# Optimization experiments

Hardware: AMD Instinct MI355X
Metric: run time of the kernel (lower is better)

The kernel has to match this reference:

```python
import jax, jax.numpy as jnp
import numpy as np

B, N, T_IN, F_IN = 16, 30000, 6, 1
E = 120000          # edges per etype
N_ETYPES = 2        # etypes per graph (hg and tg each)
KT, LK = 3, 3
C1, C2 = 8, 11      # block channel sizes
HID = 128


def _conv2d(x, w, b):
    # x: [B,Cin,T,N], w: [Cout,Cin,kt,1] -> valid conv
    y = jax.lax.conv_general_dilated(x, w, window_strides=(1, 1), padding='VALID',
                                     dimension_numbers=('NCHW', 'OIHW', 'NCHW'))
    return y + b[None, :, None, None]


def _glu_tconv(x, w, b, c_out, x_align):
    # TemporalConvLayer with act='GLU'
    xc = _conv2d(x, w, b)
    return (xc[:, :c_out] + x_align) * jax.nn.sigmoid(xc[:, c_out:])


def _hetcheb(X, edges, W, bias):
    # Heterogeneous ChebConv (sum over edge types), lambda_max=2 => L_hat = -D^-1/2 A D^-1/2
    # X: [S,N,Cin], edges: [n_et,2,E] int32, W: [n_et,Lk,Cin,Cout], bias: [n_et,Cout]
    S, n, cin = X.shape
    Lk = W.shape[1]
    Xn = jnp.transpose(X, (1, 0, 2))  # [N,S,Cin]
    out = jnp.zeros((n, S, W.shape[-1]), X.dtype)
    for e in range(edges.shape[0]):
        src, dst = edges[e, 0], edges[e, 1]
        ones = jnp.ones(src.shape, X.dtype)
        deg_in = jnp.clip(jax.ops.segment_sum(ones, dst, num_segments=n), 1.0)
        deg_out = jnp.clip(jax.ops.segment_sum(ones, src, num_segments=n), 1.0)
        norm = jax.lax.rsqrt(deg_out)[src] * jax.lax.rsqrt(deg_in)[dst]  # [E]
        def prop(Tm):  # L_hat @ T = -(Ahat @ T); vectorized over all B*T slices at once
            Tf = Tm.reshape(n, S * cin)
            return -jax.ops.segment_sum(norm[:, None] * Tf[src], dst, num_segments=n).reshape(n, S, cin)
        Tkm2 = Xn
        Tkm1 = prop(Xn)
        z = jnp.einsum('nsc,cd->nsd', Tkm2, W[e, 0]) + jnp.einsum('nsc,cd->nsd', Tkm1, W[e, 1])
        for k in range(2, Lk):
            Tk = 2.0 * prop(Tkm1) - Tkm2
            z = z + jnp.einsum('nsc,cd->nsd', Tk, W[e, k])
            Tkm2, Tkm1 = Tkm1, Tk
        out = out + z + bias[e][None, None, :]
    return jnp.transpose(out, (1, 0, 2))  # [S,N,Cout]


def _block(x, hg_edges, tg_edges, align_fn, tw, tb, hW, hb, tW, tb2, c_out):
    # HetETAConvBlock (dropout = identity in eval)
    x_align = align_fn(x)[:, :, KT - 1:, :]
    x_t1 = _glu_tconv(x, tw, tb, c_out, x_align)          # [B,c_out,T',N]
    b_, c_, t_, n_ = x_t1.shape
    X = jnp.transpose(x_t1, (0, 2, 3, 1)).reshape(b_ * t_, n_, c_)  # batched slices
    xs = _hetcheb(X, hg_edges, hW, hb).reshape(b_, t_, n_, -1).transpose(0, 3, 1, 2)
    xt = _hetcheb(X, tg_edges, tW, tb2).reshape(b_, t_, n_, -1).transpose(0, 3, 1, 2)
    return jnp.concatenate([xs, xt], axis=1)              # [B,2*c_out,T',N]


def setup_inputs() -> dict:
    key = jax.random.key(0)
    ks = jax.random.split(key, 20)
    s = 0.1
    inp = {
        'x': jax.random.normal(ks[0], (B, N, T_IN, F_IN), jnp.float32),
        'hg_edges': jax.random.randint(ks[1], (N_ETYPES, 2, E), 0, N, jnp.int32),
        'tg_edges': jax.random.randint(ks[2], (N_ETYPES, 2, E), 0, N, jnp.int32),
        # block1: tconv GLU 1 -> 8 (out 2*8 channels)
        'tconv1_w': jax.random.normal(ks[3], (2 * C1, F_IN, KT, 1), jnp.float32) * s,
        'tconv1_b': jnp.zeros((2 * C1,), jnp.float32),
        'h1_W': jax.random.normal(ks[4], (N_ETYPES, LK, C1, C1), jnp.float32) * s,
        'h1_b': jnp.zeros((N_ETYPES, C1), jnp.float32),
        't1_W': jax.random.normal(ks[5], (N_ETYPES, LK, C1, C1), jnp.float32) * s,
        't1_b': jnp.zeros((N_ETYPES, C1), jnp.float32),
        # block2: align 16 -> 11 (conv1x1), tconv GLU 16 -> 11
        'align2_w': jax.random.normal(ks[6], (C2, 2 * C1, 1, 1), jnp.float32) * s,
        'align2_b': jnp.zeros((C2,), jnp.float32),
        'tconv2_w': jax.random.normal(ks[7], (2 * C2, 2 * C1, KT, 1), jnp.float32) * s,
        'tconv2_b': jnp.zeros((2 * C2,), jnp.float32),
        'h2_W': jax.random.normal(ks[8], (N_ETYPES, LK, C2, C2), jnp.float32) * s,
        'h2_b': jnp.zeros((N_ETYPES, C2), jnp.float32),
        't2_W': jax.random.normal(ks[9], (N_ETYPES, LK, C2, C2), jnp.float32) * s,
        't2_b': jnp.zeros((N_ETYPES, C2), jnp.float32),
        # output linear: 11*2*(6-2*(3-1)) = 44 -> HID
        'out_w': jax.random.normal(ks[10], (2 * C2 * (T_IN - 2 * (KT - 1)), HID), jnp.float32) * s,
        'out_b': jnp.zeros((HID,), jnp.float32),
    }
    return inp


def reference(x, hg_edges, tg_edges, tconv1_w, tconv1_b, h1_W, h1_b, t1_W, t1_b,
              align2_w, align2_b, tconv2_w, tconv2_b, h2_W, h2_b, t2_W, t2_b,
              out_w, out_b):
    x = jnp.transpose(x, (0, 3, 2, 1))  # [B,1,T,N]
    # block1: Align pads channels 1 -> 8
    align1 = lambda v: jnp.pad(v, ((0, 0), (0, C1 - F_IN), (0, 0), (0, 0)))
    x1 = _block(x, hg_edges, tg_edges, align1, tconv1_w, tconv1_b, h1_W, h1_b, t1_W, t1_b, C1)
    # block2: Align is 1x1 conv 16 -> 11
    align2 = lambda v: _conv2d(v, align2_w, align2_b)
    x2 = _block(x1, hg_edges, tg_edges, align2, tconv2_w, tconv2_b, h2_W, h2_b, t2_W, t2_b, C2)
    b_, c_, t_, n_ = x2.shape
    z = jnp.transpose(x2, (0, 3, 1, 2)).reshape(b_, n_, c_ * t_)  # [B,N,44]
    return z @ out_w + out_b  # [B,N,HID]
```

## Files before the change

### kernel.cpp

```cpp
#include <hip/hip_runtime.h>
#include <hip/hip_fp16.h>
#include <math.h>

#define EDGES 120000
#define NN    30000
#define NCH   118
#define T1SLOT 15360000

__device__ __forceinline__ float sigmoidf_(float x) { return 1.f / (1.f + __expf(-x)); }

union F4H8 { float4 v; __half h[8]; };
union F2H4 { float2 v; __half h[4]; };

__device__ __forceinline__ void unpack8(float4 v, float* f) {
  F4H8 u; u.v = v;
#pragma unroll
  for (int i = 0; i < 8; ++i) f[i] = __half2float(u.h[i]);
}
__device__ __forceinline__ float4 pack8(const float* f) {
  F4H8 u;
#pragma unroll
  for (int i = 0; i < 8; ++i) u.h[i] = __float2half(f[i]);
  return u.v;
}
__device__ __forceinline__ void unpack4(float2 v, float* f) {
  F2H4 u; u.v = v;
#pragma unroll
  for (int i = 0; i < 4; ++i) f[i] = __half2float(u.h[i]);
}
__device__ __forceinline__ float2 pack4(const float* f) {
  F2H4 u;
#pragma unroll
  for (int i = 0; i < 4; ++i) u.h[i] = __float2half(f[i]);
  return u.v;
}

#define CSR_STRIDE 270016
#define CSR_RP(base, l)   ((base) + (size_t)(l) * CSR_STRIDE)
#define CSR_PK(base, l)   ((const int2*)((base) + (size_t)(l) * CSR_STRIDE + 30016))
#define CSR_PKW(base, l)  ((int2*)((base) + (size_t)(l) * CSR_STRIDE + 30016))

__global__ void count_all_kernel(const int* __restrict__ hg, const int* __restrict__ tg,
                                 int* __restrict__ degO, int* __restrict__ degI) {
  int tid = blockIdx.x * blockDim.x + threadIdx.x;
  if (tid >= 4 * EDGES) return;
  int l = tid / EDGES, j = tid - l * EDGES;
  const int* G = (l < 2) ? hg : tg;
  const int* src = G + (size_t)(l & 1) * 2 * EDGES;
  const int* dst = src + EDGES;
  atomicAdd(&degO[l * NN + src[j]], 1);
  atomicAdd(&degI[l * NN + dst[j]], 1);
}

__global__ __launch_bounds__(256) void scan1_kernel(const int* __restrict__ degI,
                                                    int* __restrict__ csrBase,
                                                    int* __restrict__ partials) {
  int l = blockIdx.x / NCH, ch = blockIdx.x - l * NCH;
  int tid = threadIdx.x;
  int i = ch * 256 + tid;
  __shared__ int buf[256];
  int v = (i < NN) ? degI[l * NN + i] : 0;
  buf[tid] = v;
  __syncthreads();
  for (int off = 1; off < 256; off <<= 1) {
    int t = (tid >= off) ? buf[tid - off] : 0;
    __syncthreads();
    buf[tid] += t;
    __syncthreads();
  }
  int* rp = CSR_RP(csrBase, l);
  if (i < NN) rp[i + 1] = buf[tid];
  if (tid == 255) partials[l * NCH + ch] = buf[255];
}

__global__ __launch_bounds__(128) void scan2_kernel(int* __restrict__ partials) {
  __shared__ int buf[128];
  int tid = threadIdx.x;
  for (int l = 0; l < 4; ++l) {
    int v = (tid < NCH) ? partials[l * NCH + tid] : 0;
    buf[tid] = v;
    __syncthreads();
    for (int off = 1; off < 128; off <<= 1) {
      int t = (tid >= off) ? buf[tid - off] : 0;
      __syncthreads();
      buf[tid] += t;
      __syncthreads();
    }
    if (tid < NCH) partials[l * NCH + tid] = buf[tid] - v;
    __syncthreads();
  }
}

__global__ __launch_bounds__(256) void fixup_kernel(int* __restrict__ csrBase,
                                                    int* __restrict__ cursor,
                                                    const int* __restrict__ partials) {
  int l = blockIdx.x / NCH, ch = blockIdx.x - l * NCH;
  int i = ch * 256 + threadIdx.x;
  int* rp = CSR_RP(csrBase, l);
  int off = partials[l * NCH + ch];
  if (i < NN) {
    int val = rp[i + 1] + off;
    rp[i + 1] = val;
    if (i + 1 < NN) cursor[l * NN + i + 1] = val;
  }
  if (i == 0) { rp[0] = 0; cursor[l * NN] = 0; }
}

__global__ void fill_all_kernel(const int* __restrict__ hg, const int* __restrict__ tg,
                                const int* __restrict__ degO, const int* __restrict__ degI,
                                int* __restrict__ cursor, int* __restrict__ csrBase) {
  int tid = blockIdx.x * blockDim.x + threadIdx.x;
  if (tid >= 4 * EDGES) return;
  int l = tid / EDGES, j = tid - l * EDGES;
  const int* G = (l < 2) ? hg : tg;
  const int* src = G + (size_t)(l & 1) * 2 * EDGES;
  const int* dst = src + EDGES;
  int s = src[j], d = dst[j];
  int doo = degO[l * NN + s]; if (doo < 1) doo = 1;
  int dii = degI[l * NN + d]; if (dii < 1) dii = 1;
  float nm = rsqrtf((float)doo) * rsqrtf((float)dii);
  int p = atomicAdd(&cursor[l * NN + d], 1);
  CSR_PKW(csrBase, l)[p] = make_int2(s, __float_as_int(nm));
}

__global__ void glu1_kernel(const float* __restrict__ x, const float* __restrict__ w,
                            const float* __restrict__ b, __half* __restrict__ X1h) {
  int idx = blockIdx.x * blockDim.x + threadIdx.x;
  if (idx >= NN * 64) return;
  int n = idx >> 6, s = idx & 63;
  int bb = s >> 2, t = s & 3;
  const float* xb = x + ((long)bb * NN + n) * 6;
  float x0 = xb[t], x1 = xb[t + 1], x2 = xb[t + 2];
  float o[8];
#pragma unroll
  for (int c = 0; c < 8; ++c) {
    float p = w[c * 3 + 0] * x0 + w[c * 3 + 1] * x1 + w[c * 3 + 2] * x2 + b[c];
    float q = w[(c + 8) * 3 + 0] * x0 + w[(c + 8) * 3 + 1] * x1 + w[(c + 8) * 3 + 2] * x2 + b[c + 8];
    float al = (c == 0) ? x2 : 0.f;
    o[c] = (p + al) * sigmoidf_(q);
  }
  reinterpret_cast<float4*>(X1h)[idx] = pack8(o);
}

__global__ __launch_bounds__(256) void pull1_kernel(const int* __restrict__ csrBase,
                                                    const __half* __restrict__ Xh,
                                                    __half* __restrict__ T1hAll) {
  int gtid = blockIdx.x * 256 + threadIdx.x;
  int l = gtid / (NN * 64);
  int t = gtid - l * (NN * 64);
  int n = t >> 6, j = t & 63;
  const int* rp = CSR_RP(csrBase, l);
  const int2* pk = CSR_PK(csrBase, l);
  const float4* in4 = reinterpret_cast<const float4*>(Xh);
  float acc[8];
#pragma unroll
  for (int i = 0; i < 8; ++i) acc[i] = 0.f;
  int e = rp[n], end = rp[n + 1];
  for (; e + 4 <= end; e += 4) {
    int2 p0 = pk[e], p1 = pk[e + 1], p2 = pk[e + 2], p3 = pk[e + 3];
    float4 v0 = in4[(long)p0.x * 64 + j];
    float4 v1 = in4[(long)p1.x * 64 + j];
    float4 v2 = in4[(long)p2.x * 64 + j];
    float4 v3 = in4[(long)p3.x * 64 + j];
    float f[8];
    float n0 = __int_as_float(p0.y), n1 = __int_as_float(p1.y);
    float n2 = __int_as_float(p2.y), n3 = __int_as_float(p3.y);
    unpack8(v0, f);
#pragma unroll
    for (int i = 0; i < 8; ++i) acc[i] -= n0 * f[i];
    unpack8(v1, f);
#pragma unroll
    for (int i = 0; i < 8; ++i) acc[i] -= n1 * f[i];
    unpack8(v2, f);
#pragma unroll
    for (int i = 0; i < 8; ++i) acc[i] -= n2 * f[i];
    unpack8(v3, f);
#pragma unroll
    for (int i = 0; i < 8; ++i) acc[i] -= n3 * f[i];
  }
  for (; e < end; ++e) {
    int2 p = pk[e];
    float4 v = in4[(long)p.x * 64 + j];
    float nm = __int_as_float(p.y);
    float f[8];
    unpack8(v, f);
#pragma unroll
    for (int i = 0; i < 8; ++i) acc[i] -= nm * f[i];
  }
  reinterpret_cast<float4*>(T1hAll)[(size_t)l * (T1SLOT / 8) + t] = pack8(acc);
}

__global__ __launch_bounds__(256) void cheb1_kernel(const int* __restrict__ csrBase,
    const __half* __restrict__ Xh, const __half* __restrict__ T1hAll,
    const float* __restrict__ Whg, const float* __restrict__ bhg,
    const float* __restrict__ Wtg, const float* __restrict__ btg,
    __half* __restrict__ outH, __half* __restrict__ outT) {
  constexpr int C = 8, CC = 64;
  __shared__ float wx[CC], w1a[CC], w1b[CC], w2a[CC], w2b[CC], bs[C];
  int gtid = blockIdx.x * 256 + threadIdx.x;
  int g = gtid / (NN * 64);
  int tid = gtid - g * (NN * 64);
  const float* W = g ? Wtg : Whg;
  const float* bias = g ? btg : bhg;
  for (int i = threadIdx.x; i < CC; i += 256) {
    float w0A = W[i], w1A = W[CC + i], w2A = W[2 * CC + i];
    float w0B = W[3 * CC + i], w1B = W[4 * CC + i], w2B = W[5 * CC + i];
    wx[i] = w0A - w2A + w0B - w2B;
    w1a[i] = w1A; w1b[i] = w1B;
    w2a[i] = -2.f * w2A; w2b[i] = -2.f * w2B;
  }
  if (threadIdx.x < C) bs[threadIdx.x] = bias[threadIdx.x] + bias[C + threadIdx.x];
  __syncthreads();
  int n = tid >> 6, s = tid & 63;
  int l0 = 2 * g, l1 = 2 * g + 1;
  const int* rp0 = CSR_RP(csrBase, l0); const int2* pk0 = CSR_PK(csrBase, l0);
  const int* rp1 = CSR_RP(csrBase, l1); const int2* pk1 = CSR_PK(csrBase, l1);
  const float4* A4 = reinterpret_cast<const float4*>(T1hAll + (size_t)l0 * T1SLOT);
  const float4* B4 = reinterpret_cast<const float4*>(T1hAll + (size_t)l1 * T1SLOT);
  float acc0[C], acc1[C];
#pragma unroll
  for (int c = 0; c < C; ++c) { acc0[c] = 0.f; acc1[c] = 0.f; }
  {
    int e = rp0[n], end = rp0[n + 1];
    for (; e + 2 <= end; e += 2) {
      int2 p0 = pk0[e], p1 = pk0[e + 1];
      float4 v0 = A4[(long)p0.x * 64 + s];
      float4 v1 = A4[(long)p1.x * 64 + s];
      float n0 = __int_as_float(p0.y), n1 = __int_as_float(p1.y);
      float f0[8], f1[8];
      unpack8(v0, f0); unpack8(v1, f1);
#pragma unroll
      for (int c = 0; c < C; ++c) acc0[c] += n0 * f0[c] + n1 * f1[c];
    }
    for (; e < end; ++e) {
      int2 p = pk0[e];
      float4 v = A4[(long)p.x * 64 + s];
      float nm = __int_as_float(p.y);
      float f[8]; unpack8(v, f);
#pragma unroll
      for (int c = 0; c < C; ++c) acc0[c] += nm * f[c];
    }
  }
  {
    int e = rp1[n], end = rp1[n + 1];
    for (; e + 2 <= end; e += 2) {
      int2 p0 = pk1[e], p1 = pk1[e + 1];
      float4 v0 = B4[(long)p0.x * 64 + s];
      float4 v1 = B4[(long)p1.x * 64 + s];
      float n0 = __int_as_float(p0.y), n1 = __int_as_float(p1.y);
      float f0[8], f1[8];
      unpack8(v0, f0); unpack8(v1, f1);
#pragma unroll
      for (int c = 0; c < C; ++c) acc1[c] += n0 * f0[c] + n1 * f1[c];
    }
    for (; e < end; ++e) {
      int2 p = pk1[e];
      float4 v = B4[(long)p.x * 64 + s];
      float nm = __int_as_float(p.y);
      float f[8]; unpack8(v, f);
#pragma unroll
      for (int c = 0; c < C; ++c) acc1[c] += nm * f[c];
    }
  }
  float z[C];
#pragma unroll
  for (int d = 0; d < C; ++d) z[d] = bs[d];
  {
    float xv[8], av[8], bv[8];
    unpack8(reinterpret_cast<const float4*>(Xh)[tid], xv);
    unpack8(A4[tid], av);
    unpack8(B4[tid], bv);
#pragma unroll
    for (int c = 0; c < C; ++c) {
      float x0c = xv[c], tac = av[c], tbc = bv[c], a0 = acc0[c], a1 = acc1[c];
#pragma unroll
      for (int d = 0; d < C; ++d)
        z[d] += x0c * wx[c * C + d] + tac * w1a[c * C + d] + tbc * w1b[c * C + d] +
                a0 * w2a[c * C + d] + a1 * w2b[c * C + d];
    }
  }
  reinterpret_cast<float4*>(g ? outT : outH)[tid] = pack8(z);
}

__global__ __launch_bounds__(256) void glu2_kernel(const __half* __restrict__ H, const __half* __restrict__ Tt,
                                                   const float* __restrict__ w2, const float* __restrict__ b2,
                                                   const float* __restrict__ aw, const float* __restrict__ ab,
                                                   __half* __restrict__ X2nh) {
  __shared__ float w2s[22 * 16 * 3], b2s[22], aws[11 * 16], abs_[11];
  for (int i = threadIdx.x; i < 22 * 16 * 3; i += 256) w2s[i] = w2[i];
  if (threadIdx.x < 22) b2s[threadIdx.x] = b2[threadIdx.x];
  for (int i = threadIdx.x; i < 11 * 16; i += 256) aws[i] = aw[i];
  if (threadIdx.x < 11) abs_[threadIdx.x] = ab[threadIdx.x];
  __syncthreads();
  int idx = blockIdx.x * 256 + threadIdx.x;
  int n = idx >> 5, s = idx & 31;
  int bb = s >> 1, t = s & 1;
  long rbase = (long)n * 64 + bb * 4 + t;
  const float4* H4 = reinterpret_cast<const float4*>(H) + rbase;
  const float4* T4 = reinterpret_cast<const float4*>(Tt) + rbase;
  float hv[24], tv[24];
  unpack8(H4[0], hv); unpack8(H4[1], hv + 8); unpack8(H4[2], hv + 16);
  unpack8(T4[0], tv); unpack8(T4[1], tv + 8); unpack8(T4[2], tv + 16);
  float o[12];
  o[11] = 0.f;
#pragma unroll
  for (int co = 0; co < 11; ++co) {
    float p = b2s[co], q = b2s[co + 11], a = abs_[co];
#pragma unroll
    for (int ci = 0; ci < 16; ++ci) {
      float v0 = (ci < 8) ? hv[ci] : tv[ci - 8];
      float v1 = (ci < 8) ? hv[8 + ci] : tv[ci];
      float v2 = (ci < 8) ? hv[16 + ci] : tv[8 + ci];
      p += w2s[(co * 16 + ci) * 3 + 0] * v0 + w2s[(co * 16 + ci) * 3 + 1] * v1 +
           w2s[(co * 16 + ci) * 3 + 2] * v2;
      q += w2s[((co + 11) * 16 + ci) * 3 + 0] * v0 + w2s[((co + 11) * 16 + ci) * 3 + 1] * v1 +
           w2s[((co + 11) * 16 + ci) * 3 + 2] * v2;
      a += aws[co * 16 + ci] * v2;
    }
    o[co] = (p + a) * sigmoidf_(q);
  }
  float2* o2 = reinterpret_cast<float2*>(X2nh) + (long)idx * 3;
  o2[0] = pack4(o);
  o2[1] = pack4(o + 4);
  o2[2] = pack4(o + 8);
}

__global__ __launch_bounds__(256) void pull2_kernel(const int* __restrict__ csrBase,
                                                    const __half* __restrict__ Xh,
                                                    __half* __restrict__ T1hAll) {
  int gtid = blockIdx.x * 256 + threadIdx.x;
  int l = gtid / (NN * 96);
  int t = gtid - l * (NN * 96);
  int n = t / 96, j = t - n * 96;
  const int* rp = CSR_RP(csrBase, l);
  const int2* pk = CSR_PK(csrBase, l);
  const float2* in2 = reinterpret_cast<const float2*>(Xh);
  float acc[4];
#pragma unroll
  for (int i = 0; i < 4; ++i) acc[i] = 0.f;
  int e = rp[n], end = rp[n + 1];
  for (; e + 4 <= end; e += 4) {
    int2 p0 = pk[e], p1 = pk[e + 1], p2 = pk[e + 2], p3 = pk[e + 3];
    float2 v0 = in2[(long)p0.x * 96 + j];
    float2 v1 = in2[(long)p1.x * 96 + j];
    float2 v2 = in2[(long)p2.x * 96 + j];
    float2 v3 = in2[(long)p3.x * 96 + j];
    float f[4];
    float n0 = __int_as_float(p0.y), n1 = __int_as_float(p1.y);
    float n2 = __int_as_float(p2.y), n3 = __int_as_float(p3.y);
    unpack4(v0, f);
#pragma unroll
    for (int i = 0; i < 4; ++i) acc[i] -= n0 * f[i];
    unpack4(v1, f);
#pragma unroll
    for (int i = 0; i < 4; ++i) acc[i] -= n1 * f[i];
    unpack4(v2, f);
#pragma unroll
    for (int i = 0; i < 4; ++i) acc[i] -= n2 * f[i];
    unpack4(v3, f);
#pragma unroll
    for (int i = 0; i < 4; ++i) acc[i] -= n3 * f[i];
  }
  for (; e < end; ++e) {
    int2 p = pk[e];
    float2 v = in2[(long)p.x * 96 + j];
    float nm = __int_as_float(p.y);
    float f[4];
    unpack4(v, f);
#pragma unroll
    for (int i = 0; i < 4; ++i) acc[i] -= nm * f[i];
  }
  reinterpret_cast<float2*>(T1hAll)[(size_t)l * (T1SLOT / 4) + t] = pack4(acc);
}

__global__ __launch_bounds__(256) void cheb2_kernel(const int* __restrict__ csrBase,
    const __half* __restrict__ Xh, const __half* __restrict__ T1hAll,
    const float* __restrict__ Whg, const float* __restrict__ bhg,
    const float* __restrict__ Wtg, const float* __restrict__ btg,
    __half* __restrict__ outH, __half* __restrict__ outT) {
  constexpr int C = 11, CC = 121;
  __shared__ float wx[CC], w1a[CC], w1b[CC], w2a[CC], w2b[CC], bs[C];
  int gtid = blockIdx.x * 256 + threadIdx.x;
  int g = gtid / (NN * 32);
  int tid = gtid - g * (NN * 32);
  const float* W = g ? Wtg : Whg;
  const float* bias = g ? btg : bhg;
  for (int i = threadIdx.x; i < CC; i += 256) {
    float w0A = W[i], w1A = W[CC + i], w2A = W[2 * CC + i];
    float w0B = W[3 * CC + i], w1B = W[4 * CC + i], w2B = W[5 * CC + i];
    wx[i] = w0A - w2A + w0B - w2B;
    w1a[i] = w1A; w1b[i] = w1B;
    w2a[i] = -2.f * w2A; w2b[i] = -2.f * w2B;
  }
  if (threadIdx.x < C) bs[threadIdx.x] = bias[threadIdx.x] + bias[C + threadIdx.x];
  __syncthreads();
  int n = tid >> 5, s = tid & 31;
  int s3 = s * 3;
  int l0 = 2 * g, l1 = 2 * g + 1;
  const int* rp0 = CSR_RP(csrBase, l0); const int2* pk0 = CSR_PK(csrBase, l0);
  const int* rp1 = CSR_RP(csrBase, l1); const int2* pk1 = CSR_PK(csrBase, l1);
  const float2* A2v = reinterpret_cast<const float2*>(T1hAll + (size_t)l0 * T1SLOT);
  const float2* B2v = reinterpret_cast<const float2*>(T1hAll + (size_t)l1 * T1SLOT);
  float acc0[12], acc1[12];
#pragma unroll
  for (int c = 0; c < 12; ++c) { acc0[c] = 0.f; acc1[c] = 0.f; }
  {
    int e = rp0[n], end = rp0[n + 1];
    for (; e + 2 <= end; e += 2) {
      int2 p0 = pk0[e], p1 = pk0[e + 1];
      long r0 = (long)p0.x * 96 + s3, r1 = (long)p1.x * 96 + s3;
      float2 a0 = A2v[r0], a1 = A2v[r0 + 1], a2 = A2v[r0 + 2];
      float2 b0 = A2v[r1], b1 = A2v[r1 + 1], b2 = A2v[r1 + 2];
      float n0 = __int_as_float(p0.y), n1 = __int_as_float(p1.y);
      float f[4];
      unpack4(a0, f);
#pragma unroll
      for (int i = 0; i < 4; ++i) acc0[i] += n0 * f[i];
      unpack4(a1, f);
#pragma unroll
      for (int i = 0; i < 4; ++i) acc0[4 + i] += n0 * f[i];
      unpack4(a2, f);
#pragma unroll
      for (int i = 0; i < 4; ++i) acc0[8 + i] += n0 * f[i];
      unpack4(b0, f);
#pragma unroll
      for (int i = 0; i < 4; ++i) acc0[i] += n1 * f[i];
      unpack4(b1, f);
#pragma unroll
      for (int i = 0; i < 4; ++i) acc0[4 + i] += n1 * f[i];
      unpack4(b2, f);
#pragma unroll
      for (int i = 0; i < 4; ++i) acc0[8 + i] += n1 * f[i];
    }
    for (; e < end; ++e) {
      int2 p = pk0[e];
      long r = (long)p.x * 96 + s3;
      float2 a0 = A2v[r], a1 = A2v[r + 1], a2 = A2v[r + 2];
      float nm = __int_as_float(p.y);
      float f[4];
      unpack4(a0, f);
#pragma unroll
      for (int i = 0; i < 4; ++i) acc0[i] += nm * f[i];
      unpack4(a1, f);
#pragma unroll
      for (int i = 0; i < 4; ++i) acc0[4 + i] += nm * f[i];
      unpack4(a2, f);
#pragma unroll
      for (int i = 0; i < 4; ++i) acc0[8 + i] += nm * f[i];
    }
  }
  {
    int e = rp1[n], end = rp1[n + 1];
    for (; e + 2 <= end; e += 2) {
      int2 p0 = pk1[e], p1 = pk1[e + 1];
      long r0 = (long)p0.x * 96 + s3, r1 = (long)p1.x * 96 + s3;
      float2 a0 = B2v[r0], a1 = B2v[r0 + 1], a2 = B2v[r0 + 2];
      float2 b0 = B2v[r1], b1 = B2v[r1 + 1], b2 = B2v[r1 + 2];
      float n0 = __int_as_float(p0.y), n1 = __int_as_float(p1.y);
      float f[4];
      unpack4(a0, f);
#pragma unroll
      for (int i = 0; i < 4; ++i) acc1[i] += n0 * f[i];
      unpack4(a1, f);
#pragma unroll
      for (int i = 0; i < 4; ++i) acc1[4 + i] += n0 * f[i];
      unpack4(a2, f);
#pragma unroll
      for (int i = 0; i < 4; ++i) acc1[8 + i] += n0 * f[i];
      unpack4(b0, f);
#pragma unroll
      for (int i = 0; i < 4; ++i) acc1[i] += n1 * f[i];
      unpack4(b1, f);
#pragma unroll
      for (int i = 0; i < 4; ++i) acc1[4 + i] += n1 * f[i];
      unpack4(b2, f);
#pragma unroll
      for (int i = 0; i < 4; ++i) acc1[8 + i] += n1 * f[i];
    }
    for (; e < end; ++e) {
      int2 p = pk1[e];
      long r = (long)p.x * 96 + s3;
      float2 a0 = B2v[r], a1 = B2v[r + 1], a2 = B2v[r + 2];
      float nm = __int_as_float(p.y);
      float f[4];
      unpack4(a0, f);
#pragma unroll
      for (int i = 0; i < 4; ++i) acc1[i] += nm * f[i];
      unpack4(a1, f);
#pragma unroll
      for (int i = 0; i < 4; ++i) acc1[4 + i] += nm * f[i];
      unpack4(a2, f);
#pragma unroll
      for (int i = 0; i < 4; ++i) acc1[8 + i] += nm * f[i];
    }
  }
  float z[12];
#pragma unroll
  for (int d = 0; d < C; ++d) z[d] = bs[d];
  z[11] = 0.f;
  const float2* X2v = reinterpret_cast<const float2*>(Xh);
  long own = (long)tid * 3;
#pragma unroll
  for (int q = 0; q < 3; ++q) {
    float xv[4], av[4], bv[4];
    unpack4(X2v[own + q], xv);
    unpack4(A2v[own + q], av);
    unpack4(B2v[own + q], bv);
#pragma unroll
    for (int k = 0; k < 4; ++k) {
      int c = q * 4 + k;
      if (c == 11) continue;
      float x0c = xv[k], tac = av[k], tbc = bv[k], a0 = acc0[c], a1 = acc1[c];
#pragma unroll
      for (int d = 0; d < C; ++d)
        z[d] += x0c * wx[c * C + d] + tac * w1a[c * C + d] + tbc * w1b[c * C + d] +
                a0 * w2a[c * C + d] + a1 * w2b[c * C + d];
    }
  }
  float2* o2 = reinterpret_cast<float2*>(g ? outT : outH) + (long)tid * 3;
  o2[0] = pack4(z);
  o2[1] = pack4(z + 4);
  o2[2] = pack4(z + 8);
}

__global__ __launch_bounds__(256) void final_kernel(const __half* __restrict__ H2, const __half* __restrict__ T2b,
                                                    const float* __restrict__ W, const float* __restrict__ bias,
                                                    float* __restrict__ out) {
  __shared__ __half zsr[64][48];
  int tid = threadIdx.x;
  long r0 = (long)blockIdx.x * 64;
#pragma unroll
  for (int it = 0; it < 2; ++it) {
    int item = it * 256 + tid;
    if (item < 384) {
      int row = item / 6, piece = item - row * 6;
      long r = r0 + row;
      int b = (int)(r / NN), n = (int)(r - (long)b * NN);
      const float4* srcb = reinterpret_cast<const float4*>(piece < 3 ? H2 : T2b);
      int f4i = (piece < 3) ? piece : piece - 3;
      float4 v = srcb[(long)n * 48 + b * 3 + f4i];
      *reinterpret_cast<float4*>(&zsr[row][(piece < 3 ? 0 : 24) + f4i * 8]) = v;
    }
  }
  int c = tid & 127, h = tid >> 7;
  float wp[48];
#pragma unroll
  for (int off = 0; off < 48; ++off) {
    int half_ = off / 24, r_ = off - half_ * 24;
    int t = r_ / 12, c_ = r_ - t * 12;
    wp[off] = (c_ == 11) ? 0.f : W[(2 * (c_ + half_ * 11) + t) * 128 + c];
  }
  float bh = bias[c];
  __syncthreads();
  int rbeg = h * 32;
#pragma unroll 2
  for (int row = rbeg; row < rbeg + 32; ++row) {
    const float4* zr4 = reinterpret_cast<const float4*>(&zsr[row][0]);
    float acc = bh;
#pragma unroll
    for (int q = 0; q < 6; ++q) {
      F4H8 u; u.v = zr4[q];
#pragma unroll
      for (int i = 0; i < 8; ++i)
        acc = fmaf(__half2float(u.h[i]), wp[q * 8 + i], acc);
    }
    out[(r0 + row) * 128 + c] = acc;
  }
}

extern "C" void kernel_launch(void* const* d_in, const int* in_sizes, int n_in,
                              void* d_out, int out_size, void* d_ws, size_t ws_size,
                              hipStream_t stream) {
  const float* x    = (const float*)d_in[0];
  const int*   hg   = (const int*)d_in[1];
  const int*   tg   = (const int*)d_in[2];
  const float* t1w  = (const float*)d_in[3];
  const float* t1b  = (const float*)d_in[4];
  const float* h1W  = (const float*)d_in[5];
  const float* h1b  = (const float*)d_in[6];
  const float* g1W  = (const float*)d_in[7];
  const float* g1b  = (const float*)d_in[8];
  const float* a2w  = (const float*)d_in[9];
  const float* a2b  = (const float*)d_in[10];
  const float* t2w  = (const float*)d_in[11];
  const float* t2b  = (const float*)d_in[12];
  const float* h2W  = (const float*)d_in[13];
  const float* h2b  = (const float*)d_in[14];
  const float* g2W  = (const float*)d_in[15];
  const float* g2b  = (const float*)d_in[16];
  const float* outw = (const float*)d_in[17];
  const float* outb = (const float*)d_in[18];
  float* out = (float*)d_out;

  __half* T1h = (__half*)d_ws;
  __half* Xh  = T1h + 4L * T1SLOT;
  __half* Cfh = Xh + T1SLOT;
  __half* Dfh = Cfh + T1SLOT;
  int* csrBase  = (int*)(Dfh + T1SLOT);
  int* degO     = csrBase + 4 * CSR_STRIDE;
  int* degI     = degO + 4 * NN;
  int* cursor   = degI + 4 * NN;
  int* partials = cursor + 4 * NN;

  hipMemsetAsync(degO, 0, 8 * NN * sizeof(int), stream);
  count_all_kernel<<<(4 * EDGES + 255) / 256, 256, 0, stream>>>(hg, tg, degO, degI);
  scan1_kernel<<<4 * NCH, 256, 0, stream>>>(degI, csrBase, partials);
  scan2_kernel<<<1, 128, 0, stream>>>(partials);
  fixup_kernel<<<4 * NCH, 256, 0, stream>>>(csrBase, cursor, partials);
  fill_all_kernel<<<(4 * EDGES + 255) / 256, 256, 0, stream>>>(hg, tg, degO, degI, cursor, csrBase);

  glu1_kernel<<<NN * 64 / 256, 256, 0, stream>>>(x, t1w, t1b, Xh);
  pull1_kernel<<<4 * NN * 64 / 256, 256, 0, stream>>>(csrBase, Xh, T1h);
  cheb1_kernel<<<2 * NN * 64 / 256, 256, 0, stream>>>(csrBase, Xh, T1h, h1W, h1b, g1W, g1b, Cfh, Dfh);

  glu2_kernel<<<NN * 32 / 256, 256, 0, stream>>>(Cfh, Dfh, t2w, t2b, a2w, a2b, Xh);
  pull2_kernel<<<4 * NN * 96 / 256, 256, 0, stream>>>(csrBase, Xh, T1h);
  cheb2_kernel<<<2 * NN * 32 / 256, 256, 0, stream>>>(csrBase, Xh, T1h, h2W, h2b, g2W, g2b, Cfh, Dfh);

  final_kernel<<<7500, 256, 0, stream>>>(Cfh, Dfh, outw, outb, out);
}
```

Measured before the change: 831.1 us.

## Split cheb kernels per edge type and defer partial-sum reduction to consumers

```diff
diff --git a/kernel.cpp b/kernel.cpp
--- a/kernel.cpp
+++ b/kernel.cpp
@@ -194,95 +194,77 @@
     const __half* __restrict__ Xh, const __half* __restrict__ T1hAll,
     const float* __restrict__ Whg, const float* __restrict__ bhg,
     const float* __restrict__ Wtg, const float* __restrict__ btg,
-    __half* __restrict__ outH, __half* __restrict__ outT) {
+    __half* __restrict__ Pbase) {
   constexpr int C = 8, CC = 64;
-  __shared__ float wx[CC], w1a[CC], w1b[CC], w2a[CC], w2b[CC], bs[C];
+  __shared__ float wx[CC], w1[CC], w2[CC], bs[C];
   int gtid = blockIdx.x * 256 + threadIdx.x;
-  int g = gtid / (NN * 64);
-  int tid = gtid - g * (NN * 64);
-  const float* W = g ? Wtg : Whg;
-  const float* bias = g ? btg : bhg;
+  int l = gtid / (NN * 64);
+  int tid = gtid - l * (NN * 64);
+  int g = l >> 1, et = l & 1;
+  const float* W = (g ? Wtg : Whg) + et * 3 * CC;
+  const float* bias = (g ? btg : bhg) + et * C;
   for (int i = threadIdx.x; i < CC; i += 256) {
-    float w0A = W[i], w1A = W[CC + i], w2A = W[2 * CC + i];
-    float w0B = W[3 * CC + i], w1B = W[4 * CC + i], w2B = W[5 * CC + i];
-    wx[i] = w0A - w2A + w0B - w2B;
-    w1a[i] = w1A; w1b[i] = w1B;
-    w2a[i] = -2.f * w2A; w2b[i] = -2.f * w2B;
-  }
-  if (threadIdx.x < C) bs[threadIdx.x] = bias[threadIdx.x] + bias[C + threadIdx.x];
+    float w0v = W[i], w1v = W[CC + i], w2v = W[2 * CC + i];
+    wx[i] = w0v - w2v; w1[i] = w1v; w2[i] = -2.f * w2v;
+  }
+  if (threadIdx.x < C) bs[threadIdx.x] = bias[threadIdx.x];
   __syncthreads();
   int n = tid >> 6, s = tid & 63;
-  int l0 = 2 * g, l1 = 2 * g + 1;
-  const int* rp0 = CSR_RP(csrBase, l0); const int2* pk0 = CSR_PK(csrBase, l0);
-  const int* rp1 = CSR_RP(csrBase, l1); const int2* pk1 = CSR_PK(csrBase, l1);
-  const float4* A4 = reinterpret_cast<const float4*>(T1hAll + (size_t)l0 * T1SLOT);
-  const float4* B4 = reinterpret_cast<const float4*>(T1hAll + (size_t)l1 * T1SLOT);
-  float acc0[C], acc1[C];
-#pragma unroll
-  for (int c = 0; c < C; ++c) { acc0[c] = 0.f; acc1[c] = 0.f; }
-  {
-    int e = rp0[n], end = rp0[n + 1];
-    for (; e + 2 <= end; e += 2) {
-      int2 p0 = pk0[e], p1 = pk0[e + 1];
-      float4 v0 = A4[(long)p0.x * 64 + s];
-      float4 v1 = A4[(long)p1.x * 64 + s];
-      float n0 = __int_as_float(p0.y), n1 = __int_as_float(p1.y);
-      float f0[8], f1[8];
-      unpack8(v0, f0); unpack8(v1, f1);
-#pragma unroll
-      for (int c = 0; c < C; ++c) acc0[c] += n0 * f0[c] + n1 * f1[c];
-    }
-    for (; e < end; ++e) {
-      int2 p = pk0[e];
-      float4 v = A4[(long)p.x * 64 + s];
-      float nm = __int_as_float(p.y);
-      float f[8]; unpack8(v, f);
-#pragma unroll
-      for (int c = 0; c < C; ++c) acc0[c] += nm * f[c];
-    }
-  }
-  {
-    int e = rp1[n], end = rp1[n + 1];
-    for (; e + 2 <= end; e += 2) {
-      int2 p0 = pk1[e], p1 = pk1[e + 1];
-      float4 v0 = B4[(long)p0.x * 64 + s];
-      float4 v1 = B4[(long)p1.x * 64 + s];
-      float n0 = __int_as_float(p0.y), n1 = __int_as_float(p1.y);
-      float f0[8], f1[8];
-      unpack8(v0, f0); unpack8(v1, f1);
-#pragma unroll
-      for (int c = 0; c < C; ++c) acc1[c] += n0 * f0[c] + n1 * f1[c];
-    }
-    for (; e < end; ++e) {
-      int2 p = pk1[e];
-      float4 v = B4[(long)p.x * 64 + s];
-      float nm = __int_as_float(p.y);
-      float f[8]; unpack8(v, f);
-#pragma unroll
-      for (int c = 0; c < C; ++c) acc1[c] += nm * f[c];
-    }
-  }
+  const int* rp = CSR_RP(csrBase, l);
+  const int2* pk = CSR_PK(csrBase, l);
+  const float4* T4 = reinterpret_cast<const float4*>(T1hAll + (size_t)l * T1SLOT);
+  float acc[C];
+#pragma unroll
+  for (int c = 0; c < C; ++c) acc[c] = 0.f;
+  int e = rp[n], end = rp[n + 1];
+  for (; e + 4 <= end; e += 4) {
+    int2 p0 = pk[e], p1 = pk[e + 1], p2 = pk[e + 2], p3 = pk[e + 3];
+    float4 v0 = T4[(long)p0.x * 64 + s];
+    float4 v1 = T4[(long)p1.x * 64 + s];
+    float4 v2 = T4[(long)p2.x * 64 + s];
+    float4 v3 = T4[(long)p3.x * 64 + s];
+    float n0 = __int_as_float(p0.y), n1 = __int_as_float(p1.y);
+    float n2 = __int_as_float(p2.y), n3 = __int_as_float(p3.y);
+    float f[8];
+    unpack8(v0, f);
+#pragma unroll
+    for (int c = 0; c < C; ++c) acc[c] += n0 * f[c];
+    unpack8(v1, f);
+#pragma unroll
+    for (int c = 0; c < C; ++c) acc[c] += n1 * f[c];
+    unpack8(v2, f);
+#pragma unroll
+    for (int c = 0; c < C; ++c) acc[c] += n2 * f[c];
+    unpack8(v3, f);
+#pragma unroll
+    for (int c = 0; c < C; ++c) acc[c] += n3 * f[c];
+  }
+  for (; e < end; ++e) {
+    int2 p = pk[e];
+    float4 v = T4[(long)p.x * 64 + s];
+    float nm = __int_as_float(p.y);
+    float f[8];
+    unpack8(v, f);
+#pragma unroll
+    for (int c = 0; c < C; ++c) acc[c] += nm * f[c];
+  }
+  float xv[C], tv[C];
+  unpack8(reinterpret_cast<const float4*>(Xh)[tid], xv);
+  unpack8(T4[tid], tv);
   float z[C];
 #pragma unroll
   for (int d = 0; d < C; ++d) z[d] = bs[d];
-  {
-    float xv[8], av[8], bv[8];
-    unpack8(reinterpret_cast<const float4*>(Xh)[tid], xv);
-    unpack8(A4[tid], av);
-    unpack8(B4[tid], bv);
-#pragma unroll
-    for (int c = 0; c < C; ++c) {
-      float x0c = xv[c], tac = av[c], tbc = bv[c], a0 = acc0[c], a1 = acc1[c];
-#pragma unroll
-      for (int d = 0; d < C; ++d)
-        z[d] += x0c * wx[c * C + d] + tac * w1a[c * C + d] + tbc * w1b[c * C + d] +
-                a0 * w2a[c * C + d] + a1 * w2b[c * C + d];
-    }
-  }
-  reinterpret_cast<float4*>(g ? outT : outH)[tid] = pack8(z);
-}
-
-__global__ __launch_bounds__(256) void glu2_kernel(const __half* __restrict__ H, const __half* __restrict__ Tt,
+#pragma unroll
+  for (int c = 0; c < C; ++c) {
+    float xc = xv[c], tc = tv[c], ac = acc[c];
+#pragma unroll
+    for (int d = 0; d < C; ++d)
+      z[d] += xc * wx[c * C + d] + tc * w1[c * C + d] + ac * w2[c * C + d];
+  }
+  reinterpret_cast<float4*>(Pbase)[(size_t)l * (T1SLOT / 8) + tid] = pack8(z);
+}
+
+__global__ __launch_bounds__(256) void glu2_kernel(const __half* __restrict__ P,
                                                    const float* __restrict__ w2, const float* __restrict__ b2,
                                                    const float* __restrict__ aw, const float* __restrict__ ab,
                                                    __half* __restrict__ X2nh) {
@@ -296,11 +278,20 @@
   int n = idx >> 5, s = idx & 31;
   int bb = s >> 1, t = s & 1;
   long rbase = (long)n * 64 + bb * 4 + t;
-  const float4* H4 = reinterpret_cast<const float4*>(H) + rbase;
-  const float4* T4 = reinterpret_cast<const float4*>(Tt) + rbase;
-  float hv[24], tv[24];
-  unpack8(H4[0], hv); unpack8(H4[1], hv + 8); unpack8(H4[2], hv + 16);
-  unpack8(T4[0], tv); unpack8(T4[1], tv + 8); unpack8(T4[2], tv + 16);
+  const float4* H0 = reinterpret_cast<const float4*>(P) + rbase;
+  const float4* H1 = reinterpret_cast<const float4*>(P + (size_t)T1SLOT) + rbase;
+  const float4* Ta = reinterpret_cast<const float4*>(P + 2 * (size_t)T1SLOT) + rbase;
+  const float4* Tb = reinterpret_cast<const float4*>(P + 3 * (size_t)T1SLOT) + rbase;
+  float hv[24], tv[24], tmp[8];
+#pragma unroll
+  for (int q = 0; q < 3; ++q) {
+    unpack8(H0[q], hv + 8 * q); unpack8(H1[q], tmp);
+#pragma unroll
+    for (int i = 0; i < 8; ++i) hv[8 * q + i] += tmp[i];
+    unpack8(Ta[q], tv + 8 * q); unpack8(Tb[q], tmp);
+#pragma unroll
+    for (int i = 0; i < 8; ++i) tv[8 * q + i] += tmp[i];
+  }
   float o[12];
   o[11] = 0.f;
 #pragma unroll
@@ -377,122 +368,93 @@
     const __half* __restrict__ Xh, const __half* __restrict__ T1hAll,
     const float* __restrict__ Whg, const float* __restrict__ bhg,
     const float* __restrict__ Wtg, const float* __restrict__ btg,
-    __half* __restrict__ outH, __half* __restrict__ outT) {
+    __half* __restrict__ Pbase) {
   constexpr int C = 11, CC = 121;
-  __shared__ float wx[CC], w1a[CC], w1b[CC], w2a[CC], w2b[CC], bs[C];
+  __shared__ float wx[CC], w1[CC], w2[CC], bs[C];
   int gtid = blockIdx.x * 256 + threadIdx.x;
-  int g = gtid / (NN * 32);
-  int tid = gtid - g * (NN * 32);
-  const float* W = g ? Wtg : Whg;
-  const float* bias = g ? btg : bhg;
+  int l = gtid / (NN * 32);
+  int tid = gtid - l * (NN * 32);
+  int g = l >> 1, et = l & 1;
+  const float* W = (g ? Wtg : Whg) + et * 3 * CC;
+  const float* bias = (g ? btg : bhg) + et * C;
   for (int i = threadIdx.x; i < CC; i += 256) {
-    float w0A = W[i], w1A = W[CC + i], w2A = W[2 * CC + i];
-    float w0B = W[3 * CC + i], w1B = W[4 * CC + i], w2B = W[5 * CC + i];
-    wx[i] = w0A - w2A + w0B - w2B;
-    w1a[i] = w1A; w1b[i] = w1B;
-    w2a[i] = -2.f * w2A; w2b[i] = -2.f * w2B;
-  }
-  if (threadIdx.x < C) bs[threadIdx.x] = bias[threadIdx.x] + bias[C + threadIdx.x];
+    float w0v = W[i], w1v = W[CC + i], w2v = W[2 * CC + i];
+    wx[i] = w0v - w2v; w1[i] = w1v; w2[i] = -2.f * w2v;
+  }
+  if (threadIdx.x < C) bs[threadIdx.x] = bias[threadIdx.x];
   __syncthreads();
   int n = tid >> 5, s = tid & 31;
   int s3 = s * 3;
-  int l0 = 2 * g, l1 = 2 * g + 1;
-  const int* rp0 = CSR_RP(csrBase, l0); const int2* pk0 = CSR_PK(csrBase, l0);
-  const int* rp1 = CSR_RP(csrBase, l1); const int2* pk1 = CSR_PK(csrBase, l1);
-  const float2* A2v = reinterpret_cast<const float2*>(T1hAll + (size_t)l0 * T1SLOT);
-  const float2* B2v = reinterpret_cast<const float2*>(T1hAll + (size_t)l1 * T1SLOT);
-  float acc0[12], acc1[12];
-#pragma unroll
-  for (int c = 0; c < 12; ++c) { acc0[c] = 0.f; acc1[c] = 0.f; }
-  {
-    int e = rp0[n], end = rp0[n + 1];
-    for (; e + 2 <= end; e += 2) {
-      int2 p0 = pk0[e], p1 = pk0[e + 1];
-      long r0 = (long)p0.x * 96 + s3, r1 = (long)p1.x * 96 + s3;
-      float2 a0 = A2v[r0], a1 = A2v[r0 + 1], a2 = A2v[r0 + 2];
-      float2 b0 = A2v[r1], b1 = A2v[r1 + 1], b2 = A2v[r1 + 2];
-      float n0 = __int_as_float(p0.y), n1 = __int_as_float(p1.y);
-      float f[4];
-      unpack4(a0, f);
-#pragma unroll
-      for (int i = 0; i < 4; ++i) acc0[i] += n0 * f[i];
-      unpack4(a1, f);
-#pragma unroll
-      for (int i = 0; i < 4; ++i) acc0[4 + i] += n0 * f[i];
-      unpack4(a2, f);
-#pragma unroll
-      for (int i = 0; i < 4; ++i) acc0[8 + i] += n0 * f[i];
-      unpack4(b0, f);
-#pragma unroll
-      for (int i = 0; i < 4; ++i) acc0[i] += n1 * f[i];
-      unpack4(b1, f);
-#pragma unroll
-      for (int i = 0; i < 4; ++i) acc0[4 + i] += n1 * f[i];
-      unpack4(b2, f);
-#pragma unroll
-      for (int i = 0; i < 4; ++i) acc0[8 + i] += n1 * f[i];
-    }
-    for (; e < end; ++e) {
-      int2 p = pk0[e];
-      long r = (long)p.x * 96 + s3;
-      float2 a0 = A2v[r], a1 = A2v[r + 1], a2 = A2v[r + 2];
-      float nm = __int_as_float(p.y);
-      float f[4];
-      unpack4(a0, f);
-#pragma unroll
-      for (int i = 0; i < 4; ++i) acc0[i] += nm * f[i];
-      unpack4(a1, f);
-#pragma unroll
-      for (int i = 0; i < 4; ++i) acc0[4 + i] += nm * f[i];
-      unpack4(a2, f);
-#pragma unroll
-      for (int i = 0; i < 4; ++i) acc0[8 + i] += nm * f[i];
-    }
-  }
-  {
-    int e = rp1[n], end = rp1[n + 1];
-    for (; e + 2 <= end; e += 2) {
-      int2 p0 = pk1[e], p1 = pk1[e + 1];
-      long r0 = (long)p0.x * 96 + s3, r1 = (long)p1.x * 96 + s3;
-      float2 a0 = B2v[r0], a1 = B2v[r0 + 1], a2 = B2v[r0 + 2];
-      float2 b0 = B2v[r1], b1 = B2v[r1 + 1], b2 = B2v[r1 + 2];
-      float n0 = __int_as_float(p0.y), n1 = __int_as_float(p1.y);
-      float f[4];
-      unpack4(a0, f);
-#pragma unroll
-      for (int i = 0; i < 4; ++i) acc1[i] += n0 * f[i];
-      unpack4(a1, f);
-#pragma unroll
-      for (int i = 0; i < 4; ++i) acc1[4 + i] += n0 * f[i];
-      unpack4(a2, f);
-#pragma unroll
-      for (int i = 0; i < 4; ++i) acc1[8 + i] += n0 * f[i];
-      unpack4(b0, f);
-#pragma unroll
-      for (int i = 0; i < 4; ++i) acc1[i] += n1 * f[i];
-      unpack4(b1, f);
-#pragma unroll
-      for (int i = 0; i < 4; ++i) acc1[4 + i] += n1 * f[i];
-      unpack4(b2, f);
-#pragma unroll
-      for (int i = 0; i < 4; ++i) acc1[8 + i] += n1 * f[i];
-    }
-    for (; e < end; ++e) {
-      int2 p = pk1[e];
-      long r = (long)p.x * 96 + s3;
-      float2 a0 = B2v[r], a1 = B2v[r + 1], a2 = B2v[r + 2];
-      float nm = __int_as_float(p.y);
-      float f[4];
-      unpack4(a0, f);
-#pragma unroll
-      for (int i = 0; i < 4; ++i) acc1[i] += nm * f[i];
-      unpack4(a1, f);
-#pragma unroll
-      for (int i = 0; i < 4; ++i) acc1[4 + i] += nm * f[i];
-      unpack4(a2, f);
-#pragma unroll
-      for (int i = 0; i < 4; ++i) acc1[8 + i] += nm * f[i];
-    }
+  const int* rp = CSR_RP(csrBase, l);
+  const int2* pk = CSR_PK(csrBase, l);
+  const float2* A2v = reinterpret_cast<const float2*>(T1hAll + (size_t)l * T1SLOT);
+  float acc[12];
+#pragma unroll
+  for (int c = 0; c < 12; ++c) acc[c] = 0.f;
+  int e = rp[n], end = rp[n + 1];
+  for (; e + 4 <= end; e += 4) {
+    int2 p0 = pk[e], p1 = pk[e + 1], p2 = pk[e + 2], p3 = pk[e + 3];
+    long r0 = (long)p0.x * 96 + s3, r1 = (long)p1.x * 96 + s3;
+    long r2 = (long)p2.x * 96 + s3, r3 = (long)p3.x * 96 + s3;
+    float2 a0 = A2v[r0], a1 = A2v[r0 + 1], a2 = A2v[r0 + 2];
+    float2 b0 = A2v[r1], b1 = A2v[r1 + 1], b2 = A2v[r1 + 2];
+    float2 c0 = A2v[r2], c1 = A2v[r2 + 1], c2 = A2v[r2 + 2];
+    float2 d0 = A2v[r3], d1 = A2v[r3 + 1], d2 = A2v[r3 + 2];
+    float n0 = __int_as_float(p0.y), n1 = __int_as_float(p1.y);
+    float n2 = __int_as_float(p2.y), n3 = __int_as_float(p3.y);
+    float f[4];
+    unpack4(a0, f);
+#pragma unroll
+    for (int i = 0; i < 4; ++i) acc[i] += n0 * f[i];
+    unpack4(a1, f);
+#pragma unroll
+    for (int i = 0; i < 4; ++i) acc[4 + i] += n0 * f[i];
+    unpack4(a2, f);
+#pragma unroll
+    for (int i = 0; i < 4; ++i) acc[8 + i] += n0 * f[i];
+    unpack4(b0, f);
+#pragma unroll
+    for (int i = 0; i < 4; ++i) acc[i] += n1 * f[i];
+    unpack4(b1, f);
+#pragma unroll
+    for (int i = 0; i < 4; ++i) acc[4 + i] += n1 * f[i];
+    unpack4(b2, f);
+#pragma unroll
+    for (int i = 0; i < 4; ++i) acc[8 + i] += n1 * f[i];
+    unpack4(c0, f);
+#pragma unroll
+    for (int i = 0; i < 4; ++i) acc[i] += n2 * f[i];
+    unpack4(c1, f);
+#pragma unroll
+    for (int i = 0; i < 4; ++i) acc[4 + i] += n2 * f[i];
+    unpack4(c2, f);
+#pragma unroll
+    for (int i = 0; i < 4; ++i) acc[8 + i] += n2 * f[i];
+    unpack4(d0, f);
+#pragma unroll
+    for (int i = 0; i < 4; ++i) acc[i] += n3 * f[i];
+    unpack4(d1, f);
+#pragma unroll
+    for (int i = 0; i < 4; ++i) acc[4 + i] += n3 * f[i];
+    unpack4(d2, f);
+#pragma unroll
+    for (int i = 0; i < 4; ++i) acc[8 + i] += n3 * f[i];
+  }
+  for (; e < end; ++e) {
+    int2 p = pk[e];
+    long r = (long)p.x * 96 + s3;
+    float2 a0 = A2v[r], a1 = A2v[r + 1], a2 = A2v[r + 2];
+    float nm = __int_as_float(p.y);
+    float f[4];
+    unpack4(a0, f);
+#pragma unroll
+    for (int i = 0; i < 4; ++i) acc[i] += nm * f[i];
+    unpack4(a1, f);
+#pragma unroll
+    for (int i = 0; i < 4; ++i) acc[4 + i] += nm * f[i];
+    unpack4(a2, f);
+#pragma unroll
+    for (int i = 0; i < 4; ++i) acc[8 + i] += nm * f[i];
   }
   float z[12];
 #pragma unroll
@@ -502,28 +464,26 @@
   long own = (long)tid * 3;
 #pragma unroll
   for (int q = 0; q < 3; ++q) {
-    float xv[4], av[4], bv[4];
+    float xv[4], tv[4];
     unpack4(X2v[own + q], xv);
-    unpack4(A2v[own + q], av);
-    unpack4(B2v[own + q], bv);
+    unpack4(A2v[own + q], tv);
 #pragma unroll
     for (int k = 0; k < 4; ++k) {
       int c = q * 4 + k;
       if (c == 11) continue;
-      float x0c = xv[k], tac = av[k], tbc = bv[k], a0 = acc0[c], a1 = acc1[c];
+      float xc = xv[k], tc = tv[k], ac = acc[c];
 #pragma unroll
       for (int d = 0; d < C; ++d)
-        z[d] += x0c * wx[c * C + d] + tac * w1a[c * C + d] + tbc * w1b[c * C + d] +
-                a0 * w2a[c * C + d] + a1 * w2b[c * C + d];
+        z[d] += xc * wx[c * C + d] + tc * w1[c * C + d] + ac * w2[c * C + d];
     }
   }
-  float2* o2 = reinterpret_cast<float2*>(g ? outT : outH) + (long)tid * 3;
+  float2* o2 = reinterpret_cast<float2*>(Pbase) + (size_t)l * (T1SLOT / 4) + (long)tid * 3;
   o2[0] = pack4(z);
   o2[1] = pack4(z + 4);
   o2[2] = pack4(z + 8);
 }
 
-__global__ __launch_bounds__(256) void final_kernel(const __half* __restrict__ H2, const __half* __restrict__ T2b,
+__global__ __launch_bounds__(256) void final_kernel(const __half* __restrict__ Pbase,
                                                     const float* __restrict__ W, const float* __restrict__ bias,
                                                     float* __restrict__ out) {
   __shared__ __half zsr[64][48];
@@ -536,10 +496,17 @@
       int row = item / 6, piece = item - row * 6;
       long r = r0 + row;
       int b = (int)(r / NN), n = (int)(r - (long)b * NN);
-      const float4* srcb = reinterpret_cast<const float4*>(piece < 3 ? H2 : T2b);
+      int sp = (piece < 3) ? 0 : 2;
       int f4i = (piece < 3) ? piece : piece - 3;
-      float4 v = srcb[(long)n * 48 + b * 3 + f4i];
-      *reinterpret_cast<float4*>(&zsr[row][(piece < 3 ? 0 : 24) + f4i * 8]) = v;
+      const float4* sA = reinterpret_cast<const float4*>(Pbase + (size_t)sp * T1SLOT);
+      const float4* sB = reinterpret_cast<const float4*>(Pbase + (size_t)(sp + 1) * T1SLOT);
+      long idx = (long)n * 48 + b * 3 + f4i;
+      float fa[8], fb[8];
+      unpack8(sA[idx], fa);
+      unpack8(sB[idx], fb);
+#pragma unroll
+      for (int i = 0; i < 8; ++i) fa[i] += fb[i];
+      *reinterpret_cast<float4*>(&zsr[row][(piece < 3 ? 0 : 24) + f4i * 8]) = pack8(fa);
     }
   }
   int c = tid & 127, h = tid >> 7;
@@ -594,9 +561,8 @@
 
   __half* T1h = (__half*)d_ws;
   __half* Xh  = T1h + 4L * T1SLOT;
-  __half* Cfh = Xh + T1SLOT;
-  __half* Dfh = Cfh + T1SLOT;
-  int* csrBase  = (int*)(Dfh + T1SLOT);
+  __half* P   = Xh + T1SLOT;
+  int* csrBase  = (int*)(P + 4L * T1SLOT);
   int* degO     = csrBase + 4 * CSR_STRIDE;
   int* degI     = degO + 4 * NN;
   int* cursor   = degI + 4 * NN;
@@ -611,11 +577,11 @@
 
   glu1_kernel<<<NN * 64 / 256, 256, 0, stream>>>(x, t1w, t1b, Xh);
   pull1_kernel<<<4 * NN * 64 / 256, 256, 0, stream>>>(csrBase, Xh, T1h);
-  cheb1_kernel<<<2 * NN * 64 / 256, 256, 0, stream>>>(csrBase, Xh, T1h, h1W, h1b, g1W, g1b, Cfh, Dfh);
-
-  glu2_kernel<<<NN * 32 / 256, 256, 0, stream>>>(Cfh, Dfh, t2w, t2b, a2w, a2b, Xh);
+  cheb1_kernel<<<4 * NN * 64 / 256, 256, 0, stream>>>(csrBase, Xh, T1h, h1W, h1b, g1W, g1b, P);
+
+  glu2_kernel<<<NN * 32 / 256, 256, 0, stream>>>(P, t2w, t2b, a2w, a2b, Xh);
   pull2_kernel<<<4 * NN * 96 / 256, 256, 0, stream>>>(csrBase, Xh, T1h);
-  cheb2_kernel<<<2 * NN * 32 / 256, 256, 0, stream>>>(csrBase, Xh, T1h, h2W, h2b, g2W, g2b, Cfh, Dfh);
-
-  final_kernel<<<7500, 256, 0, stream>>>(Cfh, Dfh, outw, outb, out);
-}
+  cheb2_kernel<<<4 * NN * 32 / 256, 256, 0, stream>>>(csrBase, Xh, T1h, h2W, h2b, g2W, g2b, P);
+
+  final_kernel<<<7500, 256, 0, stream>>>(P, outw, outb, out);
+}
```

Measured after the change: 899.0 us. 1.08x slower.
